# Kernel tuning notes

Hardware: AMD Instinct MI355X
Metric: run time of the kernel (lower is better)

The kernel has to match this reference:

```python
import jax, jax.numpy as jnp
import numpy as np

B, T, H, NUM_TAGS = 16, 2048, 1024, 74
RATE_HEAD, RATE_MID = 0.88, 0.7


def _make_segments(rng):
    """Build ragged word segmentation as dense index/mask tensors.

    word_idx[b, t]  : index j of the word covering char position t
    is_head[b, t]   : True iff t is the first char of its word segment
    valid_mask[b, t]: True iff t < length of utterance b
    """
    word_idx = np.zeros((B, T), dtype=np.int32)
    is_head = np.zeros((B, T), dtype=bool)
    valid = np.zeros((B, T), dtype=bool)
    for b in range(B):
        length = int(rng.integers(T // 2, T + 1))
        s, j = 0, 0
        while s < length:
            seg = int(rng.integers(1, 5))  # jieba-like segments of 1..4 chars
            seg = min(seg, length - s)
            word_idx[b, s:s + seg] = j
            is_head[b, s] = True
            valid[b, s:s + seg] = True
            s += seg
            j += 1
    return word_idx, is_head, valid


def setup_inputs() -> dict:
    key = jax.random.key(0)
    k1, k2, k3 = jax.random.split(key, 3)
    rng = np.random.default_rng(0)
    word_idx, is_head, valid = _make_segments(rng)
    return {
        "out_char": jax.random.normal(k1, (B, T, H), dtype=jnp.float32),
        "out_word": jax.random.normal(k2, (B, T, H), dtype=jnp.float32),
        "word_idx": jnp.asarray(word_idx),
        "is_head": jnp.asarray(is_head),
        "valid_mask": jnp.asarray(valid),
        "W_out": jax.random.normal(k3, (H, NUM_TAGS), dtype=jnp.float32) / np.sqrt(H),
        "b_out": jnp.zeros((NUM_TAGS,), dtype=jnp.float32),
    }


def reference(out_char, out_word, word_idx, is_head, valid_mask, W_out, b_out):
    # Feat_Merge: fused gather-scale-scatter over ragged word segments.
    # rate = rate_head on the first char of each segment, rate_mid elsewhere.
    rate = jnp.where(is_head, RATE_HEAD, RATE_MID).astype(out_char.dtype)  # [B, T]
    gathered = jnp.take_along_axis(out_word, word_idx[:, :, None], axis=1)  # [B, T, H]
    feat = gathered * rate[:, :, None] + out_char * (1.0 - rate)[:, :, None]
    feat = jnp.where(valid_mask[:, :, None], feat, 0.0)  # zeros beyond length (as in feat_B init)
    # Output tagging projection (dropout p=0 at inference)
    logits = jnp.einsum("bth,hk->btk", feat, W_out) + b_out  # [B, T, num_tags]
    return logits
```

## Files before the change

### kernel.cpp

```cpp
#include <hip/hip_runtime.h>
#include <hip/hip_bf16.h>

#define TT 2048
#define HH 1024
#define NTAGS 74
#define NPAD 80
#define CHK 64
#define NCH (HH / CHK)
#define MROWS 64

typedef __bf16 bf16x8 __attribute__((ext_vector_type(8)));
typedef float f32x4 __attribute__((ext_vector_type(4)));

__global__ __launch_bounds__(256) void prep_w_kernel(const float* __restrict__ W,
                                                     __bf16* __restrict__ Wt) {
    __shared__ float tile[64][80];
    const int k0 = blockIdx.x * 64;
    const int tid = threadIdx.x;
    for (int i = tid; i < 64 * NTAGS; i += 256) {
        int k = i / NTAGS, n = i - k * NTAGS;
        tile[k][n] = W[(k0 + k) * NTAGS + n];
    }
    __syncthreads();
    for (int i = tid; i < NPAD * 64; i += 256) {
        int n = i >> 6, kk = i & 63;
        float v = (n < NTAGS) ? tile[kk][n] : 0.0f;
        Wt[n * HH + k0 + kk] = (__bf16)v;
    }
}

__global__ __launch_bounds__(256, 2) void slu_main(const float* __restrict__ out_char,
                                                   const float* __restrict__ out_word,
                                                   const int* __restrict__ word_idx,
                                                   const int* __restrict__ is_head,
                                                   const int* __restrict__ valid_mask,
                                                   const __bf16* __restrict__ Wt,
                                                   const float* __restrict__ b_out,
                                                   float* __restrict__ out) {
    __shared__ __align__(16) char smem[45056];
    const int tid = threadIdx.x;
    const int wv = tid >> 6;
    const int lane = tid & 63;
    const int l15 = lane & 15;
    const int kgrp = lane >> 4;
    const int rowbase = blockIdx.x * MROWS;

    const int rloc = tid >> 2;
    const int q = tid & 3;
    const int r = rowbase + rloc;
    const int bq = r >> 11;
    const int widx = word_idx[r];
    const int val = valid_mask[r];
    const float rt = is_head[r] ? 0.88f : 0.70f;
    const float rate = val ? rt : 0.0f;
    const float crate = val ? (1.0f - rt) : 0.0f;
    const float* cptr = out_char + (size_t)r * HH + q * 16;
    const float* wptr = out_word + ((size_t)bq * TT + widx) * HH + q * 16;
    const int asw = (rloc & 7) << 4;
    const int awr0 = (rloc * 128 + q * 32) ^ asw;
    const int awr1 = (rloc * 128 + q * 32 + 16) ^ asw;

    const int wn0 = tid >> 3, wsb = tid & 7;
    const __bf16* wgp0 = Wt + (size_t)wn0 * HH + wsb * 8;
    const __bf16* wgp1 = wgp0 + 32 * HH;
    const __bf16* wgp2 = wgp0 + 64 * HH;
    const int wsw = (wn0 & 7) << 4;
    const int wwr0 = (wn0 * 128 + wsb * 16) ^ wsw;
    const int wwr1 = ((wn0 + 32) * 128 + wsb * 16) ^ wsw;
    const int wwr2 = ((wn0 + 64) * 128 + wsb * 16) ^ wsw;
    const bool w3 = (tid < 128);

    const int fsw = (l15 & 7) << 4;
    const int arow = wv * 16 + l15;
    int aoff[2], woff[2][5];
#pragma unroll
    for (int s = 0; s < 2; ++s) {
        aoff[s] = (arow * 128 + s * 64 + kgrp * 16) ^ fsw;
#pragma unroll
        for (int nt = 0; nt < 5; ++nt)
            woff[s][nt] = ((nt * 16 + l15) * 128 + s * 64 + kgrp * 16) ^ fsw;
    }

    f32x4 acc[5];
#pragma unroll
    for (int nt = 0; nt < 5; ++nt) acc[nt] = (f32x4){0.f, 0.f, 0.f, 0.f};

    float4 ac[4], aw[4];
    bf16x8 wreg0, wreg1, wreg2;

    {
        float4 c0[4], w0[4];
        if (val) {
#pragma unroll
            for (int i = 0; i < 4; ++i) {
                c0[i] = *(const float4*)(cptr + i * 4);
                w0[i] = *(const float4*)(wptr + i * 4);
            }
        }
        bf16x8 wr0 = *(const bf16x8*)(wgp0);
        bf16x8 wr1 = *(const bf16x8*)(wgp1);
        bf16x8 wr2 = w3 ? *(const bf16x8*)(wgp2) : (bf16x8)0;
        bf16x8 f0, f1;
        if (val) {
#pragma unroll
            for (int i = 0; i < 2; ++i) {
                f0[i * 4 + 0] = (__bf16)(w0[i].x * rate + c0[i].x * crate);
                f0[i * 4 + 1] = (__bf16)(w0[i].y * rate + c0[i].y * crate);
                f0[i * 4 + 2] = (__bf16)(w0[i].z * rate + c0[i].z * crate);
                f0[i * 4 + 3] = (__bf16)(w0[i].w * rate + c0[i].w * crate);
                f1[i * 4 + 0] = (__bf16)(w0[i + 2].x * rate + c0[i + 2].x * crate);
                f1[i * 4 + 1] = (__bf16)(w0[i + 2].y * rate + c0[i + 2].y * crate);
                f1[i * 4 + 2] = (__bf16)(w0[i + 2].z * rate + c0[i + 2].z * crate);
                f1[i * 4 + 3] = (__bf16)(w0[i + 2].w * rate + c0[i + 2].w * crate);
            }
        } else {
            f0 = (bf16x8)0; f1 = (bf16x8)0;
        }
        *(bf16x8*)(smem + awr0) = f0;
        *(bf16x8*)(smem + awr1) = f1;
        *(bf16x8*)(smem + 24576 + wwr0) = wr0;
        *(bf16x8*)(smem + 24576 + wwr1) = wr1;
        if (w3) *(bf16x8*)(smem + 24576 + wwr2) = wr2;
        if (val) {
#pragma unroll
            for (int i = 0; i < 4; ++i) {
                ac[i] = *(const float4*)(cptr + CHK + i * 4);
                aw[i] = *(const float4*)(wptr + CHK + i * 4);
            }
        }
        wreg0 = *(const bf16x8*)(wgp0 + CHK);
        wreg1 = *(const bf16x8*)(wgp1 + CHK);
        wreg2 = w3 ? *(const bf16x8*)(wgp2 + CHK) : (bf16x8)0;
    }
    __syncthreads();

    for (int ch = 0; ch < NCH; ++ch) {
        if (ch + 1 < NCH) {
            char* An = smem + ((ch + 1) % 3) * 8192;
            char* Wn = smem + 24576 + ((ch + 1) & 1) * 10240;
            bf16x8 f0, f1;
            if (val) {
#pragma unroll
                for (int i = 0; i < 2; ++i) {
                    f0[i * 4 + 0] = (__bf16)(aw[i].x * rate + ac[i].x * crate);
                    f0[i * 4 + 1] = (__bf16)(aw[i].y * rate + ac[i].y * crate);
                    f0[i * 4 + 2] = (__bf16)(aw[i].z * rate + ac[i].z * crate);
                    f0[i * 4 + 3] = (__bf16)(aw[i].w * rate + ac[i].w * crate);
                    f1[i * 4 + 0] = (__bf16)(aw[i + 2].x * rate + ac[i + 2].x * crate);
                    f1[i * 4 + 1] = (__bf16)(aw[i + 2].y * rate + ac[i + 2].y * crate);
                    f1[i * 4 + 2] = (__bf16)(aw[i + 2].z * rate + ac[i + 2].z * crate);
                    f1[i * 4 + 3] = (__bf16)(aw[i + 2].w * rate + ac[i + 2].w * crate);
                }
            } else {
                f0 = (bf16x8)0; f1 = (bf16x8)0;
            }
            *(bf16x8*)(An + awr0) = f0;
            *(bf16x8*)(An + awr1) = f1;
            *(bf16x8*)(Wn + wwr0) = wreg0;
            *(bf16x8*)(Wn + wwr1) = wreg1;
            if (w3) *(bf16x8*)(Wn + wwr2) = wreg2;
        }
        if (ch + 2 < NCH) {
            const int ko = (ch + 2) * CHK;
            if (val) {
#pragma unroll
                for (int i = 0; i < 4; ++i) {
                    ac[i] = *(const float4*)(cptr + ko + i * 4);
                    aw[i] = *(const float4*)(wptr + ko + i * 4);
                }
            }
            wreg0 = *(const bf16x8*)(wgp0 + ko);
            wreg1 = *(const bf16x8*)(wgp1 + ko);
            wreg2 = w3 ? *(const bf16x8*)(wgp2 + ko) : (bf16x8)0;
        }
        const char* Ab = smem + (ch % 3) * 8192;
        const char* Wb = smem + 24576 + (ch & 1) * 10240;
#pragma unroll
        for (int s = 0; s < 2; ++s) {
            bf16x8 a = *(const bf16x8*)(Ab + aoff[s]);
#pragma unroll
            for (int nt = 0; nt < 5; ++nt) {
                bf16x8 bw = *(const bf16x8*)(Wb + woff[s][nt]);
                acc[nt] = __builtin_amdgcn_mfma_f32_16x16x32_bf16(a, bw, acc[nt], 0, 0, 0);
            }
        }
        __syncthreads();
    }

    const int orow = rowbase + wv * 16 + kgrp * 4;
#pragma unroll
    for (int nt = 0; nt < 5; ++nt) {
        const int col = nt * 16 + l15;
        if (col < NTAGS) {
            const float bias = b_out[col];
#pragma unroll
            for (int i = 0; i < 4; ++i) {
                out[(size_t)(orow + i) * NTAGS + col] = acc[nt][i] + bias;
            }
        }
    }
}

extern "C" void kernel_launch(void* const* d_in, const int* in_sizes, int n_in,
                              void* d_out, int out_size, void* d_ws, size_t ws_size,
                              hipStream_t stream) {
    const float* out_char = (const float*)d_in[0];
    const float* out_word = (const float*)d_in[1];
    const int* word_idx = (const int*)d_in[2];
    const int* is_head = (const int*)d_in[3];
    const int* valid_mask = (const int*)d_in[4];
    const float* W_out = (const float*)d_in[5];
    const float* b_out = (const float*)d_in[6];
    float* out = (float*)d_out;
    __bf16* Wt = (__bf16*)d_ws;

    prep_w_kernel<<<HH / 64, 256, 0, stream>>>(W_out, Wt);

    const int rows = 16 * TT;
    slu_main<<<rows / MROWS, 256, 0, stream>>>(out_char, out_word, word_idx, is_head,
                                               valid_mask, Wt, b_out, out);
}
```

Baseline: 35.52 us.

## Pair front and back row tiles per block to balance ragged valid lengths

Each block now covers 128 rows with 512 threads. It pairs a 64-row tile from the front of an utterance with a mirrored 64-row tile from the back. Rows past the valid length skip their global loads, so this pairing aims to even out memory work across blocks and shrink the tail. The larger tile also spreads each W chunk load over twice as many rows. In exchange, occupancy drops to one 512-thread block per CU, and the A staging goes from triple to double buffering with a larger shared-memory footprint.

```diff
diff --git a/kernel.cpp b/kernel.cpp
--- a/kernel.cpp
+++ b/kernel.cpp
@@ -7,7 +7,8 @@
 #define NPAD 80
 #define CHK 64
 #define NCH (HH / CHK)
-#define MROWS 64
+#define MROWS 128
+#define THREADS 512
 
 typedef __bf16 bf16x8 __attribute__((ext_vector_type(8)));
 typedef float f32x4 __attribute__((ext_vector_type(4)));
@@ -29,7 +30,7 @@
     }
 }
 
-__global__ __launch_bounds__(256, 2) void slu_main(const float* __restrict__ out_char,
+__global__ __launch_bounds__(512, 1) void slu_main(const float* __restrict__ out_char,
                                                    const float* __restrict__ out_word,
                                                    const int* __restrict__ word_idx,
                                                    const int* __restrict__ is_head,
@@ -37,38 +38,40 @@
                                                    const __bf16* __restrict__ Wt,
                                                    const float* __restrict__ b_out,
                                                    float* __restrict__ out) {
-    __shared__ __align__(16) char smem[45056];
+    __shared__ __align__(16) char smem[53248];
     const int tid = threadIdx.x;
     const int wv = tid >> 6;
     const int lane = tid & 63;
     const int l15 = lane & 15;
     const int kgrp = lane >> 4;
-    const int rowbase = blockIdx.x * MROWS;
+
+    const int bid = blockIdx.x;
+    const int batch = bid >> 4;
+    const int j = bid & 15;
+    const int fb = batch * TT + j * 64;
+    const int bb = batch * TT + TT - (j + 1) * 64;
 
     const int rloc = tid >> 2;
     const int q = tid & 3;
-    const int r = rowbase + rloc;
-    const int bq = r >> 11;
+    const int r = (rloc < 64) ? (fb + rloc) : (bb + (rloc - 64));
     const int widx = word_idx[r];
     const int val = valid_mask[r];
     const float rt = is_head[r] ? 0.88f : 0.70f;
     const float rate = val ? rt : 0.0f;
     const float crate = val ? (1.0f - rt) : 0.0f;
     const float* cptr = out_char + (size_t)r * HH + q * 16;
-    const float* wptr = out_word + ((size_t)bq * TT + widx) * HH + q * 16;
+    const float* wptr = out_word + ((size_t)batch * TT + widx) * HH + q * 16;
     const int asw = (rloc & 7) << 4;
     const int awr0 = (rloc * 128 + q * 32) ^ asw;
     const int awr1 = (rloc * 128 + q * 32 + 16) ^ asw;
 
     const int wn0 = tid >> 3, wsb = tid & 7;
     const __bf16* wgp0 = Wt + (size_t)wn0 * HH + wsb * 8;
-    const __bf16* wgp1 = wgp0 + 32 * HH;
-    const __bf16* wgp2 = wgp0 + 64 * HH;
+    const __bf16* wgp1 = wgp0 + 64 * HH;
     const int wsw = (wn0 & 7) << 4;
     const int wwr0 = (wn0 * 128 + wsb * 16) ^ wsw;
-    const int wwr1 = ((wn0 + 32) * 128 + wsb * 16) ^ wsw;
-    const int wwr2 = ((wn0 + 64) * 128 + wsb * 16) ^ wsw;
-    const bool w3 = (tid < 128);
+    const int wwr1 = ((wn0 + 64) * 128 + wsb * 16) ^ wsw;
+    const bool w2 = (tid < 128);
 
     const int fsw = (l15 & 7) << 4;
     const int arow = wv * 16 + l15;
@@ -86,7 +89,7 @@
     for (int nt = 0; nt < 5; ++nt) acc[nt] = (f32x4){0.f, 0.f, 0.f, 0.f};
 
     float4 ac[4], aw[4];
-    bf16x8 wreg0, wreg1, wreg2;
+    bf16x8 wreg0, wreg1;
 
     {
         float4 c0[4], w0[4];
@@ -98,8 +101,7 @@
             }
         }
         bf16x8 wr0 = *(const bf16x8*)(wgp0);
-        bf16x8 wr1 = *(const bf16x8*)(wgp1);
-        bf16x8 wr2 = w3 ? *(const bf16x8*)(wgp2) : (bf16x8)0;
+        bf16x8 wr1 = w2 ? *(const bf16x8*)(wgp1) : (bf16x8)0;
         bf16x8 f0, f1;
         if (val) {
 #pragma unroll
@@ -118,9 +120,8 @@
         }
         *(bf16x8*)(smem + awr0) = f0;
         *(bf16x8*)(smem + awr1) = f1;
-        *(bf16x8*)(smem + 24576 + wwr0) = wr0;
-        *(bf16x8*)(smem + 24576 + wwr1) = wr1;
-        if (w3) *(bf16x8*)(smem + 24576 + wwr2) = wr2;
+        *(bf16x8*)(smem + 32768 + wwr0) = wr0;
+        if (w2) *(bf16x8*)(smem + 32768 + wwr1) = wr1;
         if (val) {
 #pragma unroll
             for (int i = 0; i < 4; ++i) {
@@ -129,15 +130,14 @@
             }
         }
         wreg0 = *(const bf16x8*)(wgp0 + CHK);
-        wreg1 = *(const bf16x8*)(wgp1 + CHK);
-        wreg2 = w3 ? *(const bf16x8*)(wgp2 + CHK) : (bf16x8)0;
+        wreg1 = w2 ? *(const bf16x8*)(wgp1 + CHK) : (bf16x8)0;
     }
     __syncthreads();
 
     for (int ch = 0; ch < NCH; ++ch) {
         if (ch + 1 < NCH) {
-            char* An = smem + ((ch + 1) % 3) * 8192;
-            char* Wn = smem + 24576 + ((ch + 1) & 1) * 10240;
+            char* An = smem + ((ch + 1) & 1) * 16384;
+            char* Wn = smem + 32768 + ((ch + 1) & 1) * 10240;
             bf16x8 f0, f1;
             if (val) {
 #pragma unroll
@@ -157,8 +157,7 @@
             *(bf16x8*)(An + awr0) = f0;
             *(bf16x8*)(An + awr1) = f1;
             *(bf16x8*)(Wn + wwr0) = wreg0;
-            *(bf16x8*)(Wn + wwr1) = wreg1;
-            if (w3) *(bf16x8*)(Wn + wwr2) = wreg2;
+            if (w2) *(bf16x8*)(Wn + wwr1) = wreg1;
         }
         if (ch + 2 < NCH) {
             const int ko = (ch + 2) * CHK;
@@ -170,11 +169,10 @@
                 }
             }
             wreg0 = *(const bf16x8*)(wgp0 + ko);
-            wreg1 = *(const bf16x8*)(wgp1 + ko);
-            wreg2 = w3 ? *(const bf16x8*)(wgp2 + ko) : (bf16x8)0;
-        }
-        const char* Ab = smem + (ch % 3) * 8192;
-        const char* Wb = smem + 24576 + (ch & 1) * 10240;
+            wreg1 = w2 ? *(const bf16x8*)(wgp1 + ko) : (bf16x8)0;
+        }
+        const char* Ab = smem + (ch & 1) * 16384;
+        const char* Wb = smem + 32768 + (ch & 1) * 10240;
 #pragma unroll
         for (int s = 0; s < 2; ++s) {
             bf16x8 a = *(const bf16x8*)(Ab + aoff[s]);
@@ -187,7 +185,8 @@
         __syncthreads();
     }
 
-    const int orow = rowbase + wv * 16 + kgrp * 4;
+    const int obase = (wv < 4) ? (fb + wv * 16) : (bb + (wv - 4) * 16);
+    const int orow = obase + kgrp * 4;
 #pragma unroll
     for (int nt = 0; nt < 5; ++nt) {
         const int col = nt * 16 + l15;
@@ -217,6 +216,6 @@
     prep_w_kernel<<<HH / 64, 256, 0, stream>>>(W_out, Wt);
 
     const int rows = 16 * TT;
-    slu_main<<<rows / MROWS, 256, 0, stream>>>(out_char, out_word, word_idx, is_head,
-                                               valid_mask, Wt, b_out, out);
+    slu_main<<<rows / MROWS, THREADS, 0, stream>>>(out_char, out_word, word_idx, is_head,
+                                                   valid_mask, Wt, b_out, out);
 }
```

Result: slower. 40.62 us (+14.3%).

## Skip fully-invalid row blocks and remap activation loads for coalescing

Applied to the files above, without the earlier changes.

Each thread now loads four rows' worth of 4-float slices (16 threads per row) instead of one row's 64 contiguous floats, so global loads across a wavefront are more contiguous per row. Blocks whose 64 rows are all beyond the utterance length write the bias directly and exit early, skipping the loads and MFMA work. The A-tile buffer goes from triple to double buffering, cutting shared memory. This adds more per-thread address registers and narrower LDS writes.

```diff
diff --git a/kernel.cpp b/kernel.cpp
--- a/kernel.cpp
+++ b/kernel.cpp
@@ -8,8 +8,10 @@
 #define CHK 64
 #define NCH (HH / CHK)
 #define MROWS 64
+#define THREADS 256
 
 typedef __bf16 bf16x8 __attribute__((ext_vector_type(8)));
+typedef __bf16 bf16x4 __attribute__((ext_vector_type(4)));
 typedef float f32x4 __attribute__((ext_vector_type(4)));
 
 __global__ __launch_bounds__(256) void prep_w_kernel(const float* __restrict__ W,
@@ -37,28 +39,44 @@
                                                    const __bf16* __restrict__ Wt,
                                                    const float* __restrict__ b_out,
                                                    float* __restrict__ out) {
-    __shared__ __align__(16) char smem[45056];
+    __shared__ __align__(16) char smem[36864];
     const int tid = threadIdx.x;
     const int wv = tid >> 6;
     const int lane = tid & 63;
     const int l15 = lane & 15;
     const int kgrp = lane >> 4;
     const int rowbase = blockIdx.x * MROWS;
-
-    const int rloc = tid >> 2;
-    const int q = tid & 3;
-    const int r = rowbase + rloc;
-    const int bq = r >> 11;
-    const int widx = word_idx[r];
-    const int val = valid_mask[r];
-    const float rt = is_head[r] ? 0.88f : 0.70f;
-    const float rate = val ? rt : 0.0f;
-    const float crate = val ? (1.0f - rt) : 0.0f;
-    const float* cptr = out_char + (size_t)r * HH + q * 16;
-    const float* wptr = out_word + ((size_t)bq * TT + widx) * HH + q * 16;
-    const int asw = (rloc & 7) << 4;
-    const int awr0 = (rloc * 128 + q * 32) ^ asw;
-    const int awr1 = (rloc * 128 + q * 32 + 16) ^ asw;
+    const int batch = rowbase >> 11;
+
+    const float* acp[4];
+    const float* awp[4];
+    float arate[4], acrate[4];
+    int aval[4], aoff[4];
+#pragma unroll
+    for (int p = 0; p < 4; ++p) {
+        const int u = tid + 256 * p;
+        const int row = u >> 4;
+        const int k16 = u & 15;
+        const int r = rowbase + row;
+        const int widx = word_idx[r];
+        const int v = valid_mask[r];
+        const float rt = is_head[r] ? 0.88f : 0.70f;
+        arate[p] = v ? rt : 0.0f;
+        acrate[p] = v ? (1.0f - rt) : 0.0f;
+        aval[p] = v;
+        acp[p] = out_char + (size_t)r * HH + k16 * 4;
+        awp[p] = out_word + ((size_t)batch * TT + widx) * HH + k16 * 4;
+        aoff[p] = (row * 128 + k16 * 8) ^ ((row & 7) << 4);
+    }
+
+    const int anyv = aval[0] | aval[1] | aval[2] | aval[3];
+    if (!__syncthreads_or(anyv)) {
+        for (int i = tid; i < MROWS * NTAGS; i += THREADS) {
+            const int rr = i / NTAGS, cc = i - rr * NTAGS;
+            out[(size_t)(rowbase + rr) * NTAGS + cc] = b_out[cc];
+        }
+        return;
+    }
 
     const int wn0 = tid >> 3, wsb = tid & 7;
     const __bf16* wgp0 = Wt + (size_t)wn0 * HH + wsb * 8;
@@ -72,13 +90,13 @@
 
     const int fsw = (l15 & 7) << 4;
     const int arow = wv * 16 + l15;
-    int aoff[2], woff[2][5];
+    int afr[2], wfr[2][5];
 #pragma unroll
     for (int s = 0; s < 2; ++s) {
-        aoff[s] = (arow * 128 + s * 64 + kgrp * 16) ^ fsw;
+        afr[s] = (arow * 128 + s * 64 + kgrp * 16) ^ fsw;
 #pragma unroll
         for (int nt = 0; nt < 5; ++nt)
-            woff[s][nt] = ((nt * 16 + l15) * 128 + s * 64 + kgrp * 16) ^ fsw;
+            wfr[s][nt] = ((nt * 16 + l15) * 128 + s * 64 + kgrp * 16) ^ fsw;
     }
 
     f32x4 acc[5];
@@ -90,42 +108,37 @@
 
     {
         float4 c0[4], w0[4];
-        if (val) {
-#pragma unroll
-            for (int i = 0; i < 4; ++i) {
-                c0[i] = *(const float4*)(cptr + i * 4);
-                w0[i] = *(const float4*)(wptr + i * 4);
+#pragma unroll
+        for (int p = 0; p < 4; ++p) {
+            if (aval[p]) {
+                c0[p] = *(const float4*)(acp[p]);
+                w0[p] = *(const float4*)(awp[p]);
             }
         }
         bf16x8 wr0 = *(const bf16x8*)(wgp0);
         bf16x8 wr1 = *(const bf16x8*)(wgp1);
         bf16x8 wr2 = w3 ? *(const bf16x8*)(wgp2) : (bf16x8)0;
-        bf16x8 f0, f1;
-        if (val) {
-#pragma unroll
-            for (int i = 0; i < 2; ++i) {
-                f0[i * 4 + 0] = (__bf16)(w0[i].x * rate + c0[i].x * crate);
-                f0[i * 4 + 1] = (__bf16)(w0[i].y * rate + c0[i].y * crate);
-                f0[i * 4 + 2] = (__bf16)(w0[i].z * rate + c0[i].z * crate);
-                f0[i * 4 + 3] = (__bf16)(w0[i].w * rate + c0[i].w * crate);
-                f1[i * 4 + 0] = (__bf16)(w0[i + 2].x * rate + c0[i + 2].x * crate);
-                f1[i * 4 + 1] = (__bf16)(w0[i + 2].y * rate + c0[i + 2].y * crate);
-                f1[i * 4 + 2] = (__bf16)(w0[i + 2].z * rate + c0[i + 2].z * crate);
-                f1[i * 4 + 3] = (__bf16)(w0[i + 2].w * rate + c0[i + 2].w * crate);
-            }
-        } else {
-            f0 = (bf16x8)0; f1 = (bf16x8)0;
-        }
-        *(bf16x8*)(smem + awr0) = f0;
-        *(bf16x8*)(smem + awr1) = f1;
-        *(bf16x8*)(smem + 24576 + wwr0) = wr0;
-        *(bf16x8*)(smem + 24576 + wwr1) = wr1;
-        if (w3) *(bf16x8*)(smem + 24576 + wwr2) = wr2;
-        if (val) {
-#pragma unroll
-            for (int i = 0; i < 4; ++i) {
-                ac[i] = *(const float4*)(cptr + CHK + i * 4);
-                aw[i] = *(const float4*)(wptr + CHK + i * 4);
+#pragma unroll
+        for (int p = 0; p < 4; ++p) {
+            bf16x4 f;
+            if (aval[p]) {
+                f[0] = (__bf16)(w0[p].x * arate[p] + c0[p].x * acrate[p]);
+                f[1] = (__bf16)(w0[p].y * arate[p] + c0[p].y * acrate[p]);
+                f[2] = (__bf16)(w0[p].z * arate[p] + c0[p].z * acrate[p]);
+                f[3] = (__bf16)(w0[p].w * arate[p] + c0[p].w * acrate[p]);
+            } else {
+                f[0] = f[1] = f[2] = f[3] = (__bf16)0.0f;
+            }
+            *(bf16x4*)(smem + aoff[p]) = f;
+        }
+        *(bf16x8*)(smem + 16384 + wwr0) = wr0;
+        *(bf16x8*)(smem + 16384 + wwr1) = wr1;
+        if (w3) *(bf16x8*)(smem + 16384 + wwr2) = wr2;
+#pragma unroll
+        for (int p = 0; p < 4; ++p) {
+            if (aval[p]) {
+                ac[p] = *(const float4*)(acp[p] + CHK);
+                aw[p] = *(const float4*)(awp[p] + CHK);
             }
         }
         wreg0 = *(const bf16x8*)(wgp0 + CHK);
@@ -136,51 +149,46 @@
 
     for (int ch = 0; ch < NCH; ++ch) {
         if (ch + 1 < NCH) {
-            char* An = smem + ((ch + 1) % 3) * 8192;
-            char* Wn = smem + 24576 + ((ch + 1) & 1) * 10240;
-            bf16x8 f0, f1;
-            if (val) {
-#pragma unroll
-                for (int i = 0; i < 2; ++i) {
-                    f0[i * 4 + 0] = (__bf16)(aw[i].x * rate + ac[i].x * crate);
-                    f0[i * 4 + 1] = (__bf16)(aw[i].y * rate + ac[i].y * crate);
-                    f0[i * 4 + 2] = (__bf16)(aw[i].z * rate + ac[i].z * crate);
-                    f0[i * 4 + 3] = (__bf16)(aw[i].w * rate + ac[i].w * crate);
-                    f1[i * 4 + 0] = (__bf16)(aw[i + 2].x * rate + ac[i + 2].x * crate);
-                    f1[i * 4 + 1] = (__bf16)(aw[i + 2].y * rate + ac[i + 2].y * crate);
-                    f1[i * 4 + 2] = (__bf16)(aw[i + 2].z * rate + ac[i + 2].z * crate);
-                    f1[i * 4 + 3] = (__bf16)(aw[i + 2].w * rate + ac[i + 2].w * crate);
+            char* An = smem + ((ch + 1) & 1) * 8192;
+            char* Wn = smem + 16384 + ((ch + 1) & 1) * 10240;
+#pragma unroll
+            for (int p = 0; p < 4; ++p) {
+                bf16x4 f;
+                if (aval[p]) {
+                    f[0] = (__bf16)(aw[p].x * arate[p] + ac[p].x * acrate[p]);
+                    f[1] = (__bf16)(aw[p].y * arate[p] + ac[p].y * acrate[p]);
+                    f[2] = (__bf16)(aw[p].z * arate[p] + ac[p].z * acrate[p]);
+                    f[3] = (__bf16)(aw[p].w * arate[p] + ac[p].w * acrate[p]);
+                } else {
+                    f[0] = f[1] = f[2] = f[3] = (__bf16)0.0f;
                 }
-            } else {
-                f0 = (bf16x8)0; f1 = (bf16x8)0;
-            }
-            *(bf16x8*)(An + awr0) = f0;
-            *(bf16x8*)(An + awr1) = f1;
+                *(bf16x4*)(An + aoff[p]) = f;
+            }
             *(bf16x8*)(Wn + wwr0) = wreg0;
             *(bf16x8*)(Wn + wwr1) = wreg1;
             if (w3) *(bf16x8*)(Wn + wwr2) = wreg2;
         }
         if (ch + 2 < NCH) {
             const int ko = (ch + 2) * CHK;
-            if (val) {
-#pragma unroll
-                for (int i = 0; i < 4; ++i) {
-                    ac[i] = *(const float4*)(cptr + ko + i * 4);
-                    aw[i] = *(const float4*)(wptr + ko + i * 4);
+#pragma unroll
+            for (int p = 0; p < 4; ++p) {
+                if (aval[p]) {
+                    ac[p] = *(const float4*)(acp[p] + ko);
+                    aw[p] = *(const float4*)(awp[p] + ko);
                 }
             }
             wreg0 = *(const bf16x8*)(wgp0 + ko);
             wreg1 = *(const bf16x8*)(wgp1 + ko);
             wreg2 = w3 ? *(const bf16x8*)(wgp2 + ko) : (bf16x8)0;
         }
-        const char* Ab = smem + (ch % 3) * 8192;
-        const char* Wb = smem + 24576 + (ch & 1) * 10240;
+        const char* Ab = smem + (ch & 1) * 8192;
+        const char* Wb = smem + 16384 + (ch & 1) * 10240;
 #pragma unroll
         for (int s = 0; s < 2; ++s) {
-            bf16x8 a = *(const bf16x8*)(Ab + aoff[s]);
+            bf16x8 a = *(const bf16x8*)(Ab + afr[s]);
 #pragma unroll
             for (int nt = 0; nt < 5; ++nt) {
-                bf16x8 bw = *(const bf16x8*)(Wb + woff[s][nt]);
+                bf16x8 bw = *(const bf16x8*)(Wb + wfr[s][nt]);
                 acc[nt] = __builtin_amdgcn_mfma_f32_16x16x32_bf16(a, bw, acc[nt], 0, 0, 0);
             }
         }
@@ -217,6 +225,6 @@
     prep_w_kernel<<<HH / 64, 256, 0, stream>>>(W_out, Wt);
 
     const int rows = 16 * TT;
-    slu_main<<<rows / MROWS, 256, 0, stream>>>(out_char, out_word, word_idx, is_head,
-                                               valid_mask, Wt, b_out, out);
+    slu_main<<<rows / MROWS, THREADS, 0, stream>>>(out_char, out_word, word_idx, is_head,
+                                                   valid_mask, Wt, b_out, out);
 }
```

Result: slower. 46.13 us (+29.9%).
